# Kernel tuning notes

Hardware: AMD Instinct MI355X
Metric: run time of the kernel (lower is better)

## Reference

```python
import jax, jax.numpy as jnp
import numpy as np

H = 16   # num_attention_heads
G = 4    # num_gqa_groups
D = 64   # head_dim = hidden // H
HIDDEN = 1024
KV_DIM = HIDDEN // H * G  # 256
EPS = 1e-5


def setup_inputs() -> dict:
    key = jax.random.key(0)
    k0, k1, k2, k3 = jax.random.split(key, 4)
    x = jax.random.normal(k0, (8, 4096, HIDDEN), dtype=jnp.float32)
    query_weight = jax.random.normal(k1, (HIDDEN, HIDDEN), dtype=jnp.float32) * 0.02
    key_weight = jax.random.normal(k2, (KV_DIM, HIDDEN), dtype=jnp.float32) * 0.02
    value_weight = jax.random.normal(k3, (KV_DIM, HIDDEN), dtype=jnp.float32) * 0.02
    return {
        "x": x,
        "query_weight": query_weight,
        "key_weight": key_weight,
        "value_weight": value_weight,
        "query_bias": jnp.zeros((HIDDEN,), jnp.float32),
        "key_bias": jnp.zeros((KV_DIM,), jnp.float32),
        "value_bias": jnp.zeros((KV_DIM,), jnp.float32),
        "layer_norm_weight": jnp.ones((HIDDEN,), jnp.float32),
        "layer_norm_bias": jnp.zeros((HIDDEN,), jnp.float32),
    }


def reference(x, query_weight, key_weight, value_weight, query_bias, key_bias,
              value_bias, layer_norm_weight, layer_norm_bias):
    b, s, _ = x.shape
    # Shared LayerNorm (q is k is v path in apply_qkv_norm)
    mu = jnp.mean(x, axis=-1, keepdims=True)
    var = jnp.mean(jnp.square(x - mu), axis=-1, keepdims=True)
    xn = (x - mu) * jax.lax.rsqrt(var + EPS) * layer_norm_weight + layer_norm_bias
    # Q/K/V projections (F.linear: x @ W.T + b)
    q = xn @ query_weight.T + query_bias           # [b, s, H*D]
    k = xn @ key_weight.T + key_bias               # [b, s, G*1*D]
    v = xn @ value_weight.T + value_bias           # [b, s, G*1*D]
    # 'b s (h d) -> b h s d'
    q = q.reshape(b, s, H, D).transpose(0, 2, 1, 3)           # [b, H, s, D]
    # 'b s (g h d) -> b h (g s) d' with h = KV_DIM//(G*D) = 1
    def kv_rearrange(t):
        t = t.reshape(b, s, G, 1, D)                          # b s g h d
        t = t.transpose(0, 3, 2, 1, 4)                        # b h g s d
        return t.reshape(b, 1, G * s, D)                      # [b, 1, G*s, D]
    return q, kv_rearrange(k), kv_rearrange(v)
```

## Files before the change

### kernel.cpp

```cpp
#include <hip/hip_runtime.h>
#include <hip/hip_bf16.h>


#define HIDDEN 1024
#define NTOK   32768

typedef __bf16 bf16x8 __attribute__((ext_vector_type(8)));
typedef float  f32x4  __attribute__((ext_vector_type(4)));

#define GLOBAL_AS(p) ((const __attribute__((address_space(1))) void*)(p))
#define LDS_AS(p)    ((__attribute__((address_space(3))) void*)(p))

__device__ __forceinline__ unsigned short f2bf(float f) {
  union { float f; unsigned int i; } x; x.f = f;
  unsigned int r = x.i + 0x7FFFu + ((x.i >> 16) & 1u);
  return (unsigned short)(r >> 16);
}

__global__ __launch_bounds__(256) void ln_cvt_kernel(
    const float* __restrict__ x,
    const float* __restrict__ gamma,
    const float* __restrict__ beta,
    const float* __restrict__ wq,
    const float* __restrict__ wk,
    const float* __restrict__ wv,
    unsigned short* __restrict__ xn,
    unsigned short* __restrict__ wb) {
  const int bid = blockIdx.x;
  const int t   = threadIdx.x;
  if (bid < NTOK) {
    const size_t base = (size_t)bid * HIDDEN;
    const float4 v = ((const float4*)(x + base))[t];
    float s  = v.x + v.y + v.z + v.w;
    float s2 = v.x*v.x + v.y*v.y + v.z*v.z + v.w*v.w;
#pragma unroll
    for (int off = 32; off >= 1; off >>= 1) {
      s  += __shfl_xor(s,  off);
      s2 += __shfl_xor(s2, off);
    }
    __shared__ float red[8];
    const int w = t >> 6;
    if ((t & 63) == 0) { red[w] = s; red[4 + w] = s2; }
    __syncthreads();
    s  = red[0] + red[1] + red[2] + red[3];
    s2 = red[4] + red[5] + red[6] + red[7];
    const float mu   = s * (1.0f / HIDDEN);
    const float rstd = rsqrtf(s2 * (1.0f / HIDDEN) - mu * mu + 1e-5f);
    const float4 g  = ((const float4*)gamma)[t];
    const float4 bb = ((const float4*)beta)[t];
    ushort4 o;
    o.x = f2bf((v.x - mu) * rstd * g.x + bb.x);
    o.y = f2bf((v.y - mu) * rstd * g.y + bb.y);
    o.z = f2bf((v.z - mu) * rstd * g.z + bb.z);
    o.w = f2bf((v.w - mu) * rstd * g.w + bb.w);
    ((ushort4*)(xn + base))[t] = o;
  } else {
    const int b2 = bid - NTOK;
    const float* src;
    int off;
    if (b2 < 1024)      { src = wq; off = b2; }
    else if (b2 < 1280) { src = wk; off = b2 - 1024; }
    else                { src = wv; off = b2 - 1280; }
    const float4 v = ((const float4*)src)[off * 256 + t];
    ushort4 o;
    o.x = f2bf(v.x); o.y = f2bf(v.y); o.z = f2bf(v.z); o.w = f2bf(v.w);
    ((ushort4*)wb)[b2 * 256 + t] = o;
  }
}

__global__ __launch_bounds__(256, 3) void qkv_gemm(
    const unsigned short* __restrict__ xn,
    const unsigned short* __restrict__ wqb,
    const float* __restrict__ bq,
    const float* __restrict__ bk,
    const float* __restrict__ bv,
    float* __restrict__ out) {
  __shared__ unsigned short lds[24576];
  unsigned short* Alds = lds;
  unsigned short* Blds = lds + 12288;

  const int bid = blockIdx.x;
  const int swz = (bid & 7) * 384 + (bid >> 3);
  const int mt  = swz / 12;
  const int nt  = swz % 12;
  const int brow = mt * 128;

  const unsigned short* wbase; const float* biasptr;
  int segcol; size_t obase; int hg;
  if (nt < 8)        { wbase = wqb + (size_t)nt * 128 * HIDDEN;                 biasptr = bq; segcol = nt * 128;        obase = 0u;        hg = 16; }
  else if (nt < 10)  { wbase = wqb + (size_t)(1024 + (nt - 8) * 128) * HIDDEN;  biasptr = bk; segcol = (nt - 8) * 128;  obase = 33554432u; hg = 4; }
  else               { wbase = wqb + (size_t)(1280 + (nt - 10) * 128) * HIDDEN; biasptr = bv; segcol = (nt - 10) * 128; obase = 41943040u; hg = 4; }

  const int t = threadIdx.x;
  const int w = t >> 6, lane = t & 63;
  const int wm = w >> 1, wn = w & 1;
  const int l15 = lane & 15, hi = lane >> 4;

  const int sr  = w * 32 + (lane >> 2);
  const int scg = ((lane & 3) ^ ((lane >> 3) & 3)) * 8;
  const unsigned short* aST = xn    + (size_t)(brow + sr) * HIDDEN + scg;
  const unsigned short* bST = wbase + (size_t)sr * HIDDEN + scg;
  const int ldsq = w * 1024;

  const int rdx  = (hi ^ ((l15 >> 1) & 3)) * 8;
  const int rowA = wm * 64 + l15;
  const int rowB = wn * 64 + l15;

  f32x4 acc[4][4];
#pragma unroll
  for (int m = 0; m < 4; ++m)
#pragma unroll
    for (int n = 0; n < 4; ++n) acc[m][n] = (f32x4){0.f, 0.f, 0.f, 0.f};
  bf16x8 a[4], b[4];

#define ST(BUF, KT) do {                                                        \
    unsigned short* _da = Alds + (BUF) * 4096 + ldsq;                           \
    unsigned short* _db = Blds + (BUF) * 4096 + ldsq;                           \
    const unsigned short* _sa = aST + (size_t)((KT) * 32);                      \
    const unsigned short* _sb = bST + (size_t)((KT) * 32);                      \
    __builtin_amdgcn_global_load_lds(GLOBAL_AS(_sa), LDS_AS(_da), 16, 0, 0);    \
    __builtin_amdgcn_global_load_lds(GLOBAL_AS(_sa + 16 * HIDDEN), LDS_AS(_da + 512), 16, 0, 0); \
    __builtin_amdgcn_global_load_lds(GLOBAL_AS(_sb), LDS_AS(_db), 16, 0, 0);    \
    __builtin_amdgcn_global_load_lds(GLOBAL_AS(_sb + 16 * HIDDEN), LDS_AS(_db + 512), 16, 0, 0); \
  } while (0)
#define RD(BUF) do { _Pragma("unroll")                                          \
    for (int m = 0; m < 4; ++m)                                                 \
      a[m] = *(const bf16x8*)(Alds + (BUF) * 4096 + (rowA + m * 16) * 32 + rdx);\
    _Pragma("unroll")                                                           \
    for (int n = 0; n < 4; ++n)                                                 \
      b[n] = *(const bf16x8*)(Blds + (BUF) * 4096 + (rowB + n * 16) * 32 + rdx);\
  } while (0)
#define MMX do { _Pragma("unroll")                                              \
    for (int m = 0; m < 4; ++m)                                                 \
      _Pragma("unroll") for (int n = 0; n < 4; ++n)                             \
        acc[m][n] = __builtin_amdgcn_mfma_f32_16x16x32_bf16(a[m], b[n], acc[m][n], 0, 0, 0); \
  } while (0)
#define PIN __builtin_amdgcn_sched_barrier(0)
#define LGKM0 asm volatile("s_waitcnt lgkmcnt(0)" ::: "memory")
#define VMW(N) asm volatile("s_waitcnt vmcnt(" #N ")" ::: "memory")
#define BAR __builtin_amdgcn_s_barrier()

#define STEP(BUF, SBUF, T) do {                                                 \
    ST(SBUF, (T) + 2); RD(BUF); PIN; LGKM0; PIN; MMX;                           \
    VMW(4); PIN; BAR; PIN;                                                      \
  } while (0)

  ST(0, 0); ST(1, 1);
  VMW(4); PIN; BAR; PIN;

  for (int T = 0; T < 30; T += 3) {
    STEP(0, 2, T);
    STEP(1, 0, T + 1);
    STEP(2, 1, T + 2);
  }
  RD(0); PIN; LGKM0; PIN; MMX; VMW(0); PIN; BAR; PIN;
  RD(1); PIN; LGKM0; PIN; MMX;
  BAR;

#undef ST
#undef RD
#undef MMX
#undef STEP
#undef LGKM0
#undef VMW
#undef BAR

  float* ep = (float*)lds;
  const int epb = w * 1344;
  const int headcol = segcol + wn * 64;
  const int gidx = headcol >> 6;
  const int tok0 = brow + wm * 64;
  const int b_ = tok0 >> 12;
  float* wout = out + obase + (size_t)(b_ * hg + gidx) * 262144u
                    + (size_t)(tok0 & 4095) * 64u;
  float biasv[4];
#pragma unroll
  for (int n = 0; n < 4; ++n) biasv[n] = biasptr[headcol + n * 16 + l15];

#pragma unroll
  for (int m = 0; m < 4; ++m) {
#pragma unroll
    for (int n = 0; n < 4; ++n)
#pragma unroll
      for (int j = 0; j < 4; ++j)
        ep[epb + (hi * 4 + j) * 84 + n * 16 + l15] = acc[m][n][j] + biasv[n];
    asm volatile("s_waitcnt lgkmcnt(0)" ::: "memory");
#pragma unroll
    for (int it = 0; it < 4; ++it) {
      const int r = it * 4 + hi;
      const float4 v = *(const float4*)(ep + epb + r * 84 + l15 * 4);
      *(float4*)(wout + (size_t)(m * 16 + r) * 64 + l15 * 4) = v;
    }
  }
#undef PIN
}

extern "C" void kernel_launch(void* const* d_in, const int* in_sizes, int n_in,
                              void* d_out, int out_size, void* d_ws, size_t ws_size,
                              hipStream_t stream) {
  const float* x  = (const float*)d_in[0];
  const float* wq = (const float*)d_in[1];
  const float* wk = (const float*)d_in[2];
  const float* wv = (const float*)d_in[3];
  const float* bq = (const float*)d_in[4];
  const float* bk = (const float*)d_in[5];
  const float* bv = (const float*)d_in[6];
  const float* g  = (const float*)d_in[7];
  const float* be = (const float*)d_in[8];
  float* out = (float*)d_out;

  unsigned short* xn = (unsigned short*)d_ws;
  unsigned short* wb = (unsigned short*)((char*)d_ws + (64u << 20));

  ln_cvt_kernel<<<NTOK + 1536, 256, 0, stream>>>(x, g, be, wq, wk, wv, xn, wb);
  qkv_gemm<<<3072, 256, 0, stream>>>(xn, wb, bq, bk, bv, out);
}
```

Baseline: 181.4 us.

## Widen GEMM tile to 128x256 with 4x8 MFMA per wave and MFMA priority

```diff
diff --git a/kernel.cpp b/kernel.cpp
--- a/kernel.cpp
+++ b/kernel.cpp
@@ -68,85 +68,89 @@
   }
 }
 
-__global__ __launch_bounds__(256, 3) void qkv_gemm(
+__global__ __launch_bounds__(256, 2) void qkv_gemm(
     const unsigned short* __restrict__ xn,
     const unsigned short* __restrict__ wqb,
     const float* __restrict__ bq,
     const float* __restrict__ bk,
     const float* __restrict__ bv,
     float* __restrict__ out) {
-  __shared__ unsigned short lds[24576];
+  __shared__ unsigned short lds[36864];
   unsigned short* Alds = lds;
   unsigned short* Blds = lds + 12288;
 
   const int bid = blockIdx.x;
-  const int swz = (bid & 7) * 384 + (bid >> 3);
-  const int mt  = swz / 12;
-  const int nt  = swz % 12;
+  const int swz = (bid & 7) * 192 + (bid >> 3);
+  const int mt  = swz & 255;
+  const int nt  = swz >> 8;
   const int brow = mt * 128;
 
   const unsigned short* wbase; const float* biasptr;
   int segcol; size_t obase; int hg;
-  if (nt < 8)        { wbase = wqb + (size_t)nt * 128 * HIDDEN;                 biasptr = bq; segcol = nt * 128;        obase = 0u;        hg = 16; }
-  else if (nt < 10)  { wbase = wqb + (size_t)(1024 + (nt - 8) * 128) * HIDDEN;  biasptr = bk; segcol = (nt - 8) * 128;  obase = 33554432u; hg = 4; }
-  else               { wbase = wqb + (size_t)(1280 + (nt - 10) * 128) * HIDDEN; biasptr = bv; segcol = (nt - 10) * 128; obase = 41943040u; hg = 4; }
+  if (nt < 4)       { wbase = wqb + (size_t)nt * 256 * HIDDEN;  biasptr = bq; segcol = nt * 256; obase = 0u;        hg = 16; }
+  else if (nt == 4) { wbase = wqb + (size_t)1024 * HIDDEN;      biasptr = bk; segcol = 0;        obase = 33554432u; hg = 4;  }
+  else              { wbase = wqb + (size_t)1280 * HIDDEN;      biasptr = bv; segcol = 0;        obase = 41943040u; hg = 4;  }
 
   const int t = threadIdx.x;
   const int w = t >> 6, lane = t & 63;
   const int wm = w >> 1, wn = w & 1;
   const int l15 = lane & 15, hi = lane >> 4;
 
-  const int sr  = w * 32 + (lane >> 2);
   const int scg = ((lane & 3) ^ ((lane >> 3) & 3)) * 8;
-  const unsigned short* aST = xn    + (size_t)(brow + sr) * HIDDEN + scg;
-  const unsigned short* bST = wbase + (size_t)sr * HIDDEN + scg;
-  const int ldsq = w * 1024;
+  const unsigned short* aST = xn    + (size_t)(brow + w * 32 + (lane >> 2)) * HIDDEN + scg;
+  const unsigned short* bST = wbase + (size_t)(w * 64 + (lane >> 2)) * HIDDEN + scg;
+  const int aQ = w * 1024;
+  const int bQ = w * 2048;
 
   const int rdx  = (hi ^ ((l15 >> 1) & 3)) * 8;
-  const int rowA = wm * 64 + l15;
-  const int rowB = wn * 64 + l15;
-
-  f32x4 acc[4][4];
+  const int rowA = wm * 64  + l15;
+  const int rowB = wn * 128 + l15;
+
+  f32x4 acc[4][8];
 #pragma unroll
   for (int m = 0; m < 4; ++m)
 #pragma unroll
-    for (int n = 0; n < 4; ++n) acc[m][n] = (f32x4){0.f, 0.f, 0.f, 0.f};
-  bf16x8 a[4], b[4];
-
-#define ST(BUF, KT) do {                                                        \
-    unsigned short* _da = Alds + (BUF) * 4096 + ldsq;                           \
-    unsigned short* _db = Blds + (BUF) * 4096 + ldsq;                           \
+    for (int n = 0; n < 8; ++n) acc[m][n] = (f32x4){0.f, 0.f, 0.f, 0.f};
+  bf16x8 a[4], b[8];
+
+#define ST(R, KT) do {                                                          \
+    unsigned short* _da = Alds + (R) * 4096 + aQ;                               \
+    unsigned short* _db = Blds + (R) * 8192 + bQ;                               \
     const unsigned short* _sa = aST + (size_t)((KT) * 32);                      \
     const unsigned short* _sb = bST + (size_t)((KT) * 32);                      \
     __builtin_amdgcn_global_load_lds(GLOBAL_AS(_sa), LDS_AS(_da), 16, 0, 0);    \
     __builtin_amdgcn_global_load_lds(GLOBAL_AS(_sa + 16 * HIDDEN), LDS_AS(_da + 512), 16, 0, 0); \
-    __builtin_amdgcn_global_load_lds(GLOBAL_AS(_sb), LDS_AS(_db), 16, 0, 0);    \
-    __builtin_amdgcn_global_load_lds(GLOBAL_AS(_sb + 16 * HIDDEN), LDS_AS(_db + 512), 16, 0, 0); \
-  } while (0)
-#define RD(BUF) do { _Pragma("unroll")                                          \
+    _Pragma("unroll")                                                           \
+    for (int i = 0; i < 4; ++i)                                                 \
+      __builtin_amdgcn_global_load_lds(GLOBAL_AS(_sb + (size_t)i * 16 * HIDDEN), \
+                                       LDS_AS(_db + i * 512), 16, 0, 0);        \
+  } while (0)
+#define RD(R) do { _Pragma("unroll")                                            \
     for (int m = 0; m < 4; ++m)                                                 \
-      a[m] = *(const bf16x8*)(Alds + (BUF) * 4096 + (rowA + m * 16) * 32 + rdx);\
+      a[m] = *(const bf16x8*)(Alds + (R) * 4096 + (rowA + m * 16) * 32 + rdx);  \
     _Pragma("unroll")                                                           \
-    for (int n = 0; n < 4; ++n)                                                 \
-      b[n] = *(const bf16x8*)(Blds + (BUF) * 4096 + (rowB + n * 16) * 32 + rdx);\
-  } while (0)
-#define MMX do { _Pragma("unroll")                                              \
-    for (int m = 0; m < 4; ++m)                                                 \
-      _Pragma("unroll") for (int n = 0; n < 4; ++n)                             \
+    for (int n = 0; n < 8; ++n)                                                 \
+      b[n] = *(const bf16x8*)(Blds + (R) * 8192 + (rowB + n * 16) * 32 + rdx);  \
+  } while (0)
+#define MMX do {                                                                \
+    __builtin_amdgcn_s_setprio(1);                                              \
+    _Pragma("unroll") for (int m = 0; m < 4; ++m)                               \
+      _Pragma("unroll") for (int n = 0; n < 8; ++n)                             \
         acc[m][n] = __builtin_amdgcn_mfma_f32_16x16x32_bf16(a[m], b[n], acc[m][n], 0, 0, 0); \
+    __builtin_amdgcn_s_setprio(0);                                              \
   } while (0)
 #define PIN __builtin_amdgcn_sched_barrier(0)
 #define LGKM0 asm volatile("s_waitcnt lgkmcnt(0)" ::: "memory")
 #define VMW(N) asm volatile("s_waitcnt vmcnt(" #N ")" ::: "memory")
 #define BAR __builtin_amdgcn_s_barrier()
 
-#define STEP(BUF, SBUF, T) do {                                                 \
-    ST(SBUF, (T) + 2); RD(BUF); PIN; LGKM0; PIN; MMX;                           \
-    VMW(4); PIN; BAR; PIN;                                                      \
+#define STEP(R, SR, T) do {                                                     \
+    ST(SR, (T) + 2); RD(R); PIN; LGKM0; PIN; MMX;                               \
+    VMW(6); PIN; BAR; PIN;                                                      \
   } while (0)
 
   ST(0, 0); ST(1, 1);
-  VMW(4); PIN; BAR; PIN;
+  VMW(6); PIN; BAR; PIN;
 
   for (int T = 0; T < 30; T += 3) {
     STEP(0, 2, T);
@@ -155,44 +159,46 @@
   }
   RD(0); PIN; LGKM0; PIN; MMX; VMW(0); PIN; BAR; PIN;
   RD(1); PIN; LGKM0; PIN; MMX;
-  BAR;
+  LGKM0; PIN; BAR; PIN;
 
 #undef ST
 #undef RD
 #undef MMX
 #undef STEP
+
+  float* ep = (float*)lds;
+  const int epb = w * 2112;
+  const int tok0 = brow + wm * 64;
+  float biasv[8];
+#pragma unroll
+  for (int n = 0; n < 8; ++n) biasv[n] = biasptr[segcol + wn * 128 + n * 16 + l15];
+
+#pragma unroll
+  for (int m = 0; m < 4; ++m) {
+#pragma unroll
+    for (int n = 0; n < 8; ++n)
+#pragma unroll
+      for (int j = 0; j < 4; ++j)
+        ep[epb + (hi * 4 + j) * 132 + n * 16 + l15] = acc[m][n][j] + biasv[n];
+    LGKM0;
+    PIN;
+#pragma unroll
+    for (int pass = 0; pass < 8; ++pass) {
+      const int r = pass * 2 + (lane >> 5);
+      const int c = (lane & 31) * 4;
+      const float4 v = *(const float4*)(ep + epb + r * 132 + c);
+      const int ncol = segcol + wn * 128 + c;
+      const int g = ncol >> 6, d = ncol & 63;
+      const int token = tok0 + m * 16 + r;
+      const int b_ = token >> 12, s = token & 4095;
+      *(float4*)(out + obase + (size_t)(b_ * hg + g) * 262144u
+                     + (size_t)s * 64u + d) = v;
+    }
+  }
+#undef PIN
 #undef LGKM0
 #undef VMW
 #undef BAR
-
-  float* ep = (float*)lds;
-  const int epb = w * 1344;
-  const int headcol = segcol + wn * 64;
-  const int gidx = headcol >> 6;
-  const int tok0 = brow + wm * 64;
-  const int b_ = tok0 >> 12;
-  float* wout = out + obase + (size_t)(b_ * hg + gidx) * 262144u
-                    + (size_t)(tok0 & 4095) * 64u;
-  float biasv[4];
-#pragma unroll
-  for (int n = 0; n < 4; ++n) biasv[n] = biasptr[headcol + n * 16 + l15];
-
-#pragma unroll
-  for (int m = 0; m < 4; ++m) {
-#pragma unroll
-    for (int n = 0; n < 4; ++n)
-#pragma unroll
-      for (int j = 0; j < 4; ++j)
-        ep[epb + (hi * 4 + j) * 84 + n * 16 + l15] = acc[m][n][j] + biasv[n];
-    asm volatile("s_waitcnt lgkmcnt(0)" ::: "memory");
-#pragma unroll
-    for (int it = 0; it < 4; ++it) {
-      const int r = it * 4 + hi;
-      const float4 v = *(const float4*)(ep + epb + r * 84 + l15 * 4);
-      *(float4*)(wout + (size_t)(m * 16 + r) * 64 + l15 * 4) = v;
-    }
-  }
-#undef PIN
 }
 
 extern "C" void kernel_launch(void* const* d_in, const int* in_sizes, int n_in,
@@ -213,5 +219,5 @@
   unsigned short* wb = (unsigned short*)((char*)d_ws + (64u << 20));
 
   ln_cvt_kernel<<<NTOK + 1536, 256, 0, stream>>>(x, g, be, wq, wk, wv, xn, wb);
-  qkv_gemm<<<3072, 256, 0, stream>>>(xn, wb, bq, bk, bv, out);
-}
+  qkv_gemm<<<1536, 256, 0, stream>>>(xn, wb, bq, bk, bv, out);
+}
```

Result: faster. 171.3 us (-5.5%).
